# Kernel optimization log

Hardware: AMD Instinct MI355X
Metric: run time of the kernel (lower is better)

The kernel has to match this reference:

```python
import jax, jax.numpy as jnp
import numpy as np

B, S, D = 4, 4096, 768
E, SLOTS = 16, 1  # n_experts, slots_per_expert
H = 4 * D


def setup_inputs() -> dict:
    key = jax.random.key(0)
    k = jax.random.split(key, 6)
    scale1 = 1.0 / np.sqrt(D)
    scale2 = 1.0 / np.sqrt(H)
    return {
        "x": jax.random.normal(k[0], (B, S, D), dtype=jnp.float32),
        "phi": jax.random.normal(k[1], (D, E * SLOTS), dtype=jnp.float32),
        "W1": jax.random.normal(k[2], (E, D, H), dtype=jnp.float32) * scale1,
        "b1": jnp.zeros((E, H), dtype=jnp.float32),
        "W2": jax.random.normal(k[3], (E, H, D), dtype=jnp.float32) * scale2,
        "b2": jnp.zeros((E, D), dtype=jnp.float32),
    }


def reference(x, phi, W1, b1, W2, b2):
    # logits: [B, S, E*SLOTS]
    logits = jnp.einsum("bsd,dn->bsn", x, phi)
    dispatch_weights = jax.nn.softmax(logits, axis=-1)  # over slots
    combine_weights = jax.nn.softmax(logits, axis=1)    # over sequence
    # xs: [B, E*SLOTS, D] = dispatch^T @ x
    xs = jnp.einsum("bsn,bsd->bnd", dispatch_weights, x)
    xs = xs.reshape(B, E, SLOTS, D)
    # per-expert FFN, batched over experts: GELU (exact, as torch nn.GELU default)
    h = jnp.einsum("bepd,edh->beph", xs, W1) + b1[None, :, None, :]
    h = jax.nn.gelu(h, approximate=False)
    ys = jnp.einsum("beph,ehd->bepd", h, W2) + b2[None, :, None, :]
    ys = ys.reshape(B, E * SLOTS, D)
    # combine: [B, S, D]
    y = jnp.einsum("bsn,bnd->bsd", combine_weights, ys)
    return y
```

## Files before the change

kernel.cpp:

```cpp
#include <hip/hip_runtime.h>
#include <math.h>

constexpr int B = 4, S = 4096, D = 768, E = 16, N = 16, H = 3072;
constexpr int SCH = 32;
constexpr int NSCH = S / SCH;
constexpr int HL = 96;
constexpr int NHC = H / HL;
constexpr int LBLK = 32;
constexpr int LPB = S / LBLK;

constexpr size_t OFF_LOG  = 0;
constexpr size_t OFF_DW   = OFF_LOG + (size_t)B * S * N;
constexpr size_t OFF_PCM  = OFF_DW + (size_t)B * S * N;
constexpr size_t OFF_PCS  = OFF_PCM + (size_t)B * LPB * N;
constexpr size_t OFF_CMAX = OFF_PCS + (size_t)B * LPB * N;
constexpr size_t OFF_CSUM = OFF_CMAX + (size_t)B * N;
constexpr size_t OFF_XSP  = OFF_CSUM + (size_t)B * N;
constexpr size_t OFF_XS   = OFF_XSP + (size_t)B * NSCH * N * D;
constexpr size_t OFF_YSP  = OFF_XS + (size_t)B * N * D;
constexpr size_t OFF_YS   = OFF_YSP + (size_t)NHC * B * E * D;

__device__ __forceinline__ void fma4(float4& a, float s, const float4& w) {
    a.x = fmaf(s, w.x, a.x);
    a.y = fmaf(s, w.y, a.y);
    a.z = fmaf(s, w.z, a.z);
    a.w = fmaf(s, w.w, a.w);
}

__global__ __launch_bounds__(256) void k_logits(const float* __restrict__ x,
                                                const float* __restrict__ phi,
                                                float* __restrict__ logits,
                                                float* __restrict__ dw,
                                                float* __restrict__ pcm,
                                                float* __restrict__ pcs) {
    __shared__ float ph[16][D];
    __shared__ float rm[16][16], rs[16][16];
    const int t = threadIdx.x;
    const int blk = blockIdx.x;
    const int b = blk / LPB;
    const int s0 = (blk % LPB) * LBLK;

#pragma unroll
    for (int i = 0; i < 12; ++i) {
        const int idx = i * 1024 + t * 4;
        const float4 v = *reinterpret_cast<const float4*>(phi + idx);
        const int d0 = idx >> 4;
        const int n0 = idx & 15;
        ph[n0 + 0][d0] = v.x;
        ph[n0 + 1][d0] = v.y;
        ph[n0 + 2][d0] = v.z;
        ph[n0 + 3][d0] = v.w;
    }
    __syncthreads();

    const int gid = t >> 4;
    const int ln = t & 15;
    const int s = s0 + gid * 2;
    const float* xr0 = x + ((size_t)b * S + s) * D;
    const float* xr1 = xr0 + D;

    float4 a0[12], a1[12];
#pragma unroll
    for (int j = 0; j < 12; ++j) {
        a0[j] = *reinterpret_cast<const float4*>(xr0 + j * 64 + ln * 4);
        a1[j] = *reinterpret_cast<const float4*>(xr1 + j * 64 + ln * 4);
    }
    float p0[16], p1[16];
#pragma unroll
    for (int n = 0; n < 16; ++n) {
        float q0 = 0.f, q1 = 0.f;
#pragma unroll
        for (int j = 0; j < 12; ++j) {
            const float4 pv = *reinterpret_cast<const float4*>(&ph[n][j * 64 + ln * 4]);
            q0 = fmaf(a0[j].x, pv.x, q0); q1 = fmaf(a1[j].x, pv.x, q1);
            q0 = fmaf(a0[j].y, pv.y, q0); q1 = fmaf(a1[j].y, pv.y, q1);
            q0 = fmaf(a0[j].z, pv.z, q0); q1 = fmaf(a1[j].z, pv.z, q1);
            q0 = fmaf(a0[j].w, pv.w, q0); q1 = fmaf(a1[j].w, pv.w, q1);
        }
        p0[n] = q0; p1[n] = q1;
    }
#pragma unroll
    for (int m = 1; m < 16; m <<= 1) {
#pragma unroll
        for (int n = 0; n < 16; ++n) {
            p0[n] += __shfl_xor(p0[n], m, 64);
            p1[n] += __shfl_xor(p1[n], m, 64);
        }
    }
    float m0 = -1e30f, m1 = -1e30f;
#pragma unroll
    for (int n = 0; n < 16; ++n) { m0 = fmaxf(m0, p0[n]); m1 = fmaxf(m1, p1[n]); }
    float su0 = 0.f, su1 = 0.f;
#pragma unroll
    for (int n = 0; n < 16; ++n) { su0 += __expf(p0[n] - m0); su1 += __expf(p1[n] - m1); }
    const size_t o0 = ((size_t)b * S + s) * N + ln;
    logits[o0] = p0[ln];
    logits[o0 + N] = p1[ln];
    dw[o0] = __expf(p0[ln] - m0) / su0;
    dw[o0 + N] = __expf(p1[ln] - m1) / su1;

    const float mm = fmaxf(p0[ln], p1[ln]);
    const float ss = __expf(p0[ln] - mm) + __expf(p1[ln] - mm);
    rm[gid][ln] = mm;
    rs[gid][ln] = ss;
    __syncthreads();
    if (t < 16) {
        float M = -1e30f;
#pragma unroll
        for (int g = 0; g < 16; ++g) M = fmaxf(M, rm[g][t]);
        float SS = 0.f;
#pragma unroll
        for (int g = 0; g < 16; ++g) SS += rs[g][t] * __expf(rm[g][t] - M);
        pcm[blk * 16 + t] = M;
        pcs[blk * 16 + t] = SS;
    }
}

__global__ __launch_bounds__(192) void k_xsp(const float* __restrict__ x,
                                             const float* __restrict__ dw,
                                             float* __restrict__ xsp) {
    const int blk = blockIdx.x;
    const int b = blk / NSCH;
    const int c = blk % NSCH;
    const int t = threadIdx.x;
    const int d = t * 4;
    float4 a[16];
#pragma unroll
    for (int n = 0; n < 16; ++n) a[n] = float4{0.f, 0.f, 0.f, 0.f};
    const float* xb = x + ((size_t)b * S + (size_t)c * SCH) * D + d;
    const float* dwb = dw + ((size_t)b * S + (size_t)c * SCH) * N;
#pragma unroll 2
    for (int s = 0; s < SCH; ++s) {
        const float4 xv = *reinterpret_cast<const float4*>(xb + (size_t)s * D);
#pragma unroll
        for (int n = 0; n < 16; ++n) {
            const float w = dwb[s * N + n];
            a[n].x = fmaf(w, xv.x, a[n].x);
            a[n].y = fmaf(w, xv.y, a[n].y);
            a[n].z = fmaf(w, xv.z, a[n].z);
            a[n].w = fmaf(w, xv.w, a[n].w);
        }
    }
    float* o = xsp + (size_t)blk * N * D + d;
#pragma unroll
    for (int n = 0; n < 16; ++n)
        *reinterpret_cast<float4*>(o + (size_t)n * D) = a[n];
}

__global__ __launch_bounds__(256) void k_xsred_cmerge(const float* __restrict__ xsp,
                                                      float* __restrict__ xs,
                                                      const float* __restrict__ pcm,
                                                      const float* __restrict__ pcs,
                                                      float* __restrict__ cmax,
                                                      float* __restrict__ csum) {
    const int t = threadIdx.x;
    if (blockIdx.x < 192) {
        const int i = blockIdx.x * 256 + t;
        const int b = i / (N * D);
        const int rem = i % (N * D);
        const float* p = xsp + (size_t)b * NSCH * N * D + rem;
        float sum = 0.f;
#pragma unroll 4
        for (int c = 0; c < NSCH; ++c) sum += p[(size_t)c * N * D];
        xs[i] = sum;
    } else if (t < 64) {
        const int b = t >> 4, n = t & 15;
        float M = -1e30f;
#pragma unroll 8
        for (int c = 0; c < LPB; ++c) M = fmaxf(M, pcm[((size_t)b * LPB + c) * 16 + n]);
        float SS = 0.f;
#pragma unroll 8
        for (int c = 0; c < LPB; ++c)
            SS += pcs[((size_t)b * LPB + c) * 16 + n] * __expf(pcm[((size_t)b * LPB + c) * 16 + n] - M);
        cmax[b * 16 + n] = M;
        csum[b * 16 + n] = SS;
    }
}

__global__ __launch_bounds__(384) void k_ffn(const float* __restrict__ xs,
                                             const float* __restrict__ W1,
                                             const float* __restrict__ b1,
                                             const float* __restrict__ W2,
                                             float* __restrict__ ysp) {
    __shared__ __align__(16) float xs_lds[D][4];
    __shared__ __align__(16) float red_lds[16][HL][4];
    __shared__ __align__(16) float h_lds[HL][4];

    const int t = threadIdx.x;
    const int e = blockIdx.x / NHC;
    const int hc = blockIdx.x % NHC;
    const int h0 = hc * HL;

    for (int idx = t; idx < D; idx += 384) {
#pragma unroll
        for (int b = 0; b < 4; ++b)
            xs_lds[idx][b] = xs[((size_t)b * N + e) * D + idx];
    }
    __syncthreads();

    {
        const int c4 = (t % 24) * 4;
        const int q = t / 24;
        float4 h0a{0,0,0,0}, h1a{0,0,0,0}, h2a{0,0,0,0}, h3a{0,0,0,0};
        const float* w1p = W1 + ((size_t)e * D + (size_t)q * 48) * H + h0 + c4;
#pragma unroll 8
        for (int dd = 0; dd < 48; ++dd) {
            const float4 w = *reinterpret_cast<const float4*>(w1p + (size_t)dd * H);
            const float* xv = &xs_lds[q * 48 + dd][0];
            const float x0 = xv[0], x1 = xv[1], x2 = xv[2], x3 = xv[3];
            h0a.x = fmaf(x0, w.x, h0a.x); h0a.y = fmaf(x0, w.y, h0a.y);
            h0a.z = fmaf(x0, w.z, h0a.z); h0a.w = fmaf(x0, w.w, h0a.w);
            h1a.x = fmaf(x1, w.x, h1a.x); h1a.y = fmaf(x1, w.y, h1a.y);
            h1a.z = fmaf(x1, w.z, h1a.z); h1a.w = fmaf(x1, w.w, h1a.w);
            h2a.x = fmaf(x2, w.x, h2a.x); h2a.y = fmaf(x2, w.y, h2a.y);
            h2a.z = fmaf(x2, w.z, h2a.z); h2a.w = fmaf(x2, w.w, h2a.w);
            h3a.x = fmaf(x3, w.x, h3a.x); h3a.y = fmaf(x3, w.y, h3a.y);
            h3a.z = fmaf(x3, w.z, h3a.z); h3a.w = fmaf(x3, w.w, h3a.w);
        }
        *reinterpret_cast<float4*>(&red_lds[q][c4 + 0][0]) = float4{h0a.x, h1a.x, h2a.x, h3a.x};
        *reinterpret_cast<float4*>(&red_lds[q][c4 + 1][0]) = float4{h0a.y, h1a.y, h2a.y, h3a.y};
        *reinterpret_cast<float4*>(&red_lds[q][c4 + 2][0]) = float4{h0a.z, h1a.z, h2a.z, h3a.z};
        *reinterpret_cast<float4*>(&red_lds[q][c4 + 3][0]) = float4{h0a.w, h1a.w, h2a.w, h3a.w};
    }
    __syncthreads();

    const int dgrp = t % 192;
    const int kq = t / 192;
    const float* w2p = W2 + ((size_t)e * H + h0 + (size_t)kq * 48) * D + dgrp * 4;
    float4 wpre[8];
#pragma unroll
    for (int i = 0; i < 8; ++i)
        wpre[i] = *reinterpret_cast<const float4*>(w2p + (size_t)i * D);

    {
        const int col = t >> 2, b = t & 3;
        float s = 0.f;
#pragma unroll
        for (int q = 0; q < 16; ++q) s += red_lds[q][col][b];
        s += b1[(size_t)e * H + h0 + col];
        s = 0.5f * s * (1.0f + erff(s * 0.70710678118654752f));
        h_lds[col][b] = s;
    }
    __syncthreads();

    float4 acc[4];
#pragma unroll
    for (int b = 0; b < 4; ++b) acc[b] = float4{0.f, 0.f, 0.f, 0.f};

#pragma unroll
    for (int kk = 0; kk < 8; ++kk) {
        const float4 hv = *reinterpret_cast<const float4*>(&h_lds[kq * 48 + kk][0]);
        fma4(acc[0], hv.x, wpre[kk]);
        fma4(acc[1], hv.y, wpre[kk]);
        fma4(acc[2], hv.z, wpre[kk]);
        fma4(acc[3], hv.w, wpre[kk]);
    }
#pragma unroll 8
    for (int kk = 8; kk < 48; ++kk) {
        const float4 w = *reinterpret_cast<const float4*>(w2p + (size_t)kk * D);
        const float4 hv = *reinterpret_cast<const float4*>(&h_lds[kq * 48 + kk][0]);
        fma4(acc[0], hv.x, w);
        fma4(acc[1], hv.y, w);
        fma4(acc[2], hv.z, w);
        fma4(acc[3], hv.w, w);
    }

    float4* pbuf = reinterpret_cast<float4*>(&xs_lds[0][0]);
    __syncthreads();
    if (kq == 1) {
#pragma unroll
        for (int b = 0; b < 4; ++b) pbuf[dgrp * 4 + b] = acc[b];
    }
    __syncthreads();
    if (kq == 0) {
#pragma unroll
        for (int b = 0; b < 4; ++b) {
            const float4 u = pbuf[dgrp * 4 + b];
            float4 r{acc[b].x + u.x, acc[b].y + u.y, acc[b].z + u.z, acc[b].w + u.w};
            *reinterpret_cast<float4*>(ysp + (((size_t)hc * B + b) * E + e) * D + dgrp * 4) = r;
        }
    }
}

__global__ __launch_bounds__(256) void k_ysred(const float* __restrict__ ysp,
                                               const float* __restrict__ b2,
                                               float* __restrict__ ys) {
    const int i4 = blockIdx.x * 256 + threadIdx.x;
    const int rem4 = i4 % (E * D / 4);
    float4 v = *reinterpret_cast<const float4*>(b2 + (size_t)rem4 * 4);
#pragma unroll 8
    for (int p = 0; p < NHC; ++p) {
        const float4 u = *reinterpret_cast<const float4*>(ysp + (size_t)p * B * E * D + (size_t)i4 * 4);
        v.x += u.x; v.y += u.y; v.z += u.z; v.w += u.w;
    }
    *reinterpret_cast<float4*>(ys + (size_t)i4 * 4) = v;
}

__global__ __launch_bounds__(192) void k_combine(const float* __restrict__ logits,
                                                 const float* __restrict__ cmax,
                                                 const float* __restrict__ csum,
                                                 const float* __restrict__ ys,
                                                 float* __restrict__ y) {
    const int blk = blockIdx.x;
    const int b = blk / (S / 8);
    const int s0 = (blk % (S / 8)) * 8;
    const int t = threadIdx.x;
    const int d4 = t * 4;

    float4 ysr[16];
    float cm[16], ci[16];
#pragma unroll
    for (int n = 0; n < 16; ++n) {
        ysr[n] = *reinterpret_cast<const float4*>(ys + ((size_t)b * N + n) * D + d4);
        cm[n] = cmax[b * N + n];
        ci[n] = 1.0f / csum[b * N + n];
    }
#pragma unroll
    for (int r = 0; r < 8; ++r) {
        const int s = s0 + r;
        const float* lrow = logits + ((size_t)b * S + s) * N;
        float4 acc{0, 0, 0, 0};
#pragma unroll
        for (int n = 0; n < 16; ++n) {
            const float cw = __expf(lrow[n] - cm[n]) * ci[n];
            acc.x = fmaf(cw, ysr[n].x, acc.x);
            acc.y = fmaf(cw, ysr[n].y, acc.y);
            acc.z = fmaf(cw, ysr[n].z, acc.z);
            acc.w = fmaf(cw, ysr[n].w, acc.w);
        }
        *reinterpret_cast<float4*>(y + ((size_t)b * S + s) * D + d4) = acc;
    }
}

extern "C" void kernel_launch(void* const* d_in, const int* in_sizes, int n_in,
                              void* d_out, int out_size, void* d_ws, size_t ws_size,
                              hipStream_t stream) {
    const float* x   = (const float*)d_in[0];
    const float* phi = (const float*)d_in[1];
    const float* W1  = (const float*)d_in[2];
    const float* b1  = (const float*)d_in[3];
    const float* W2  = (const float*)d_in[4];
    const float* b2  = (const float*)d_in[5];
    float* y = (float*)d_out;
    float* ws = (float*)d_ws;

    float* logits = ws + OFF_LOG;
    float* dw     = ws + OFF_DW;
    float* pcm    = ws + OFF_PCM;
    float* pcs    = ws + OFF_PCS;
    float* cmax   = ws + OFF_CMAX;
    float* csum   = ws + OFF_CSUM;
    float* xsp    = ws + OFF_XSP;
    float* xs     = ws + OFF_XS;
    float* ysp    = ws + OFF_YSP;
    float* ys     = ws + OFF_YS;

    k_logits<<<B * LPB, 256, 0, stream>>>(x, phi, logits, dw, pcm, pcs);
    k_xsp<<<B * NSCH, 192, 0, stream>>>(x, dw, xsp);
    k_xsred_cmerge<<<193, 256, 0, stream>>>(xsp, xs, pcm, pcs, cmax, csum);
    k_ffn<<<E * NHC, 384, 0, stream>>>(xs, W1, b1, W2, ysp);
    k_ysred<<<48, 256, 0, stream>>>(ysp, b2, ys);
    k_combine<<<B * (S / 8), 192, 0, stream>>>(logits, cmax, csum, ys, y);
}
```

Before: 153.8 us.

## Fuse logits and dispatch-weighted x reduction into one kernel; restructure FFN thread mapping

Merges the logits/softmax kernel with the per-chunk dispatch^T·x reduction. Each block stages its 32 rows of x in LDS and keeps the dispatch weights there, so x is read from global memory once instead of twice and the dw buffer round trip is removed. It also remaps the FFN kernel so each thread computes two column groups over a shorter K slice, using a 32-way reduction in phase 1 and a 4-way reduction in phase 2. The cost is a large LDS footprint in the fused kernel (about 150 KB) and idle threads during the xsp phase, which may reduce occupancy.

```diff
diff --git a/kernel.cpp b/kernel.cpp
--- a/kernel.cpp
+++ b/kernel.cpp
@@ -2,21 +2,18 @@
 #include <math.h>
 
 constexpr int B = 4, S = 4096, D = 768, E = 16, N = 16, H = 3072;
-constexpr int SCH = 32;
-constexpr int NSCH = S / SCH;
 constexpr int HL = 96;
 constexpr int NHC = H / HL;
 constexpr int LBLK = 32;
 constexpr int LPB = S / LBLK;
 
 constexpr size_t OFF_LOG  = 0;
-constexpr size_t OFF_DW   = OFF_LOG + (size_t)B * S * N;
-constexpr size_t OFF_PCM  = OFF_DW + (size_t)B * S * N;
+constexpr size_t OFF_PCM  = OFF_LOG + (size_t)B * S * N;
 constexpr size_t OFF_PCS  = OFF_PCM + (size_t)B * LPB * N;
 constexpr size_t OFF_CMAX = OFF_PCS + (size_t)B * LPB * N;
 constexpr size_t OFF_CSUM = OFF_CMAX + (size_t)B * N;
 constexpr size_t OFF_XSP  = OFF_CSUM + (size_t)B * N;
-constexpr size_t OFF_XS   = OFF_XSP + (size_t)B * NSCH * N * D;
+constexpr size_t OFF_XS   = OFF_XSP + (size_t)B * LPB * N * D;
 constexpr size_t OFF_YSP  = OFF_XS + (size_t)B * N * D;
 constexpr size_t OFF_YS   = OFF_YSP + (size_t)NHC * B * E * D;
 
@@ -27,13 +24,15 @@
     a.w = fmaf(s, w.w, a.w);
 }
 
-__global__ __launch_bounds__(256) void k_logits(const float* __restrict__ x,
-                                                const float* __restrict__ phi,
-                                                float* __restrict__ logits,
-                                                float* __restrict__ dw,
-                                                float* __restrict__ pcm,
-                                                float* __restrict__ pcs) {
+__global__ __launch_bounds__(256) void k_lx(const float* __restrict__ x,
+                                            const float* __restrict__ phi,
+                                            float* __restrict__ logits,
+                                            float* __restrict__ xsp,
+                                            float* __restrict__ pcm,
+                                            float* __restrict__ pcs) {
     __shared__ float ph[16][D];
+    __shared__ float xr[LBLK][D + 4];
+    __shared__ float dwl[LBLK][16];
     __shared__ float rm[16][16], rs[16][16];
     const int t = threadIdx.x;
     const int blk = blockIdx.x;
@@ -51,19 +50,25 @@
         ph[n0 + 2][d0] = v.z;
         ph[n0 + 3][d0] = v.w;
     }
+    const float* xsrc = x + ((size_t)b * S + s0) * D;
+#pragma unroll
+    for (int i = 0; i < 24; ++i) {
+        const int idx = i * 256 + t;
+        const int r = idx / 192, c = idx % 192;
+        *reinterpret_cast<float4*>(&xr[r][c * 4]) =
+            *reinterpret_cast<const float4*>(xsrc + (size_t)idx * 4);
+    }
     __syncthreads();
 
     const int gid = t >> 4;
     const int ln = t & 15;
-    const int s = s0 + gid * 2;
-    const float* xr0 = x + ((size_t)b * S + s) * D;
-    const float* xr1 = xr0 + D;
+    const int r0 = gid * 2, r1 = r0 + 1;
 
     float4 a0[12], a1[12];
 #pragma unroll
     for (int j = 0; j < 12; ++j) {
-        a0[j] = *reinterpret_cast<const float4*>(xr0 + j * 64 + ln * 4);
-        a1[j] = *reinterpret_cast<const float4*>(xr1 + j * 64 + ln * 4);
+        a0[j] = *reinterpret_cast<const float4*>(&xr[r0][j * 64 + ln * 4]);
+        a1[j] = *reinterpret_cast<const float4*>(&xr[r1][j * 64 + ln * 4]);
     }
     float p0[16], p1[16];
 #pragma unroll
@@ -93,17 +98,17 @@
     float su0 = 0.f, su1 = 0.f;
 #pragma unroll
     for (int n = 0; n < 16; ++n) { su0 += __expf(p0[n] - m0); su1 += __expf(p1[n] - m1); }
-    const size_t o0 = ((size_t)b * S + s) * N + ln;
+    const size_t o0 = ((size_t)b * S + s0 + r0) * N + ln;
     logits[o0] = p0[ln];
     logits[o0 + N] = p1[ln];
-    dw[o0] = __expf(p0[ln] - m0) / su0;
-    dw[o0 + N] = __expf(p1[ln] - m1) / su1;
+    dwl[r0][ln] = __expf(p0[ln] - m0) / su0;
+    dwl[r1][ln] = __expf(p1[ln] - m1) / su1;
 
     const float mm = fmaxf(p0[ln], p1[ln]);
-    const float ss = __expf(p0[ln] - mm) + __expf(p1[ln] - mm);
     rm[gid][ln] = mm;
-    rs[gid][ln] = ss;
-    __syncthreads();
+    rs[gid][ln] = __expf(p0[ln] - mm) + __expf(p1[ln] - mm);
+    __syncthreads();
+
     if (t < 16) {
         float M = -1e30f;
 #pragma unroll
@@ -114,37 +119,29 @@
         pcm[blk * 16 + t] = M;
         pcs[blk * 16 + t] = SS;
     }
-}
-
-__global__ __launch_bounds__(192) void k_xsp(const float* __restrict__ x,
-                                             const float* __restrict__ dw,
-                                             float* __restrict__ xsp) {
-    const int blk = blockIdx.x;
-    const int b = blk / NSCH;
-    const int c = blk % NSCH;
-    const int t = threadIdx.x;
-    const int d = t * 4;
-    float4 a[16];
-#pragma unroll
-    for (int n = 0; n < 16; ++n) a[n] = float4{0.f, 0.f, 0.f, 0.f};
-    const float* xb = x + ((size_t)b * S + (size_t)c * SCH) * D + d;
-    const float* dwb = dw + ((size_t)b * S + (size_t)c * SCH) * N;
-#pragma unroll 2
-    for (int s = 0; s < SCH; ++s) {
-        const float4 xv = *reinterpret_cast<const float4*>(xb + (size_t)s * D);
-#pragma unroll
-        for (int n = 0; n < 16; ++n) {
-            const float w = dwb[s * N + n];
-            a[n].x = fmaf(w, xv.x, a[n].x);
-            a[n].y = fmaf(w, xv.y, a[n].y);
-            a[n].z = fmaf(w, xv.z, a[n].z);
-            a[n].w = fmaf(w, xv.w, a[n].w);
-        }
-    }
-    float* o = xsp + (size_t)blk * N * D + d;
-#pragma unroll
-    for (int n = 0; n < 16; ++n)
-        *reinterpret_cast<float4*>(o + (size_t)n * D) = a[n];
+
+    if (t < 192) {
+        const int d4 = t * 4;
+        float4 a[16];
+#pragma unroll
+        for (int n = 0; n < 16; ++n) a[n] = float4{0.f, 0.f, 0.f, 0.f};
+#pragma unroll 4
+        for (int s = 0; s < LBLK; ++s) {
+            const float4 xv = *reinterpret_cast<const float4*>(&xr[s][d4]);
+#pragma unroll
+            for (int n = 0; n < 16; ++n) {
+                const float w = dwl[s][n];
+                a[n].x = fmaf(w, xv.x, a[n].x);
+                a[n].y = fmaf(w, xv.y, a[n].y);
+                a[n].z = fmaf(w, xv.z, a[n].z);
+                a[n].w = fmaf(w, xv.w, a[n].w);
+            }
+        }
+        float* o = xsp + (size_t)blk * N * D + d4;
+#pragma unroll
+        for (int n = 0; n < 16; ++n)
+            *reinterpret_cast<float4*>(o + (size_t)n * D) = a[n];
+    }
 }
 
 __global__ __launch_bounds__(256) void k_xsred_cmerge(const float* __restrict__ xsp,
@@ -158,10 +155,10 @@
         const int i = blockIdx.x * 256 + t;
         const int b = i / (N * D);
         const int rem = i % (N * D);
-        const float* p = xsp + (size_t)b * NSCH * N * D + rem;
+        const float* p = xsp + (size_t)b * LPB * N * D + rem;
         float sum = 0.f;
 #pragma unroll 4
-        for (int c = 0; c < NSCH; ++c) sum += p[(size_t)c * N * D];
+        for (int c = 0; c < LPB; ++c) sum += p[(size_t)c * N * D];
         xs[i] = sum;
     } else if (t < 64) {
         const int b = t >> 4, n = t & 15;
@@ -183,7 +180,7 @@
                                              const float* __restrict__ W2,
                                              float* __restrict__ ysp) {
     __shared__ __align__(16) float xs_lds[D][4];
-    __shared__ __align__(16) float red_lds[16][HL][4];
+    __shared__ __align__(16) float red[32][HL][4];
     __shared__ __align__(16) float h_lds[HL][4];
 
     const int t = threadIdx.x;
@@ -199,85 +196,92 @@
     __syncthreads();
 
     {
-        const int c4 = (t % 24) * 4;
-        const int q = t / 24;
-        float4 h0a{0,0,0,0}, h1a{0,0,0,0}, h2a{0,0,0,0}, h3a{0,0,0,0};
-        const float* w1p = W1 + ((size_t)e * D + (size_t)q * 48) * H + h0 + c4;
-#pragma unroll 8
-        for (int dd = 0; dd < 48; ++dd) {
-            const float4 w = *reinterpret_cast<const float4*>(w1p + (size_t)dd * H);
-            const float* xv = &xs_lds[q * 48 + dd][0];
+        const int q = t / 12;
+        const int cg = t % 12;
+        const int c4a = cg * 4, c4b = 48 + cg * 4;
+        float4 aA[4], aB[4];
+#pragma unroll
+        for (int b = 0; b < 4; ++b) { aA[b] = float4{0,0,0,0}; aB[b] = float4{0,0,0,0}; }
+        const float* w1p = W1 + ((size_t)e * D + (size_t)q * 24) * H + h0;
+#pragma unroll 8
+        for (int dd = 0; dd < 24; ++dd) {
+            const float* row = w1p + (size_t)dd * H;
+            const float4 wa = *reinterpret_cast<const float4*>(row + c4a);
+            const float4 wb = *reinterpret_cast<const float4*>(row + c4b);
+            const float* xv = &xs_lds[q * 24 + dd][0];
             const float x0 = xv[0], x1 = xv[1], x2 = xv[2], x3 = xv[3];
-            h0a.x = fmaf(x0, w.x, h0a.x); h0a.y = fmaf(x0, w.y, h0a.y);
-            h0a.z = fmaf(x0, w.z, h0a.z); h0a.w = fmaf(x0, w.w, h0a.w);
-            h1a.x = fmaf(x1, w.x, h1a.x); h1a.y = fmaf(x1, w.y, h1a.y);
-            h1a.z = fmaf(x1, w.z, h1a.z); h1a.w = fmaf(x1, w.w, h1a.w);
-            h2a.x = fmaf(x2, w.x, h2a.x); h2a.y = fmaf(x2, w.y, h2a.y);
-            h2a.z = fmaf(x2, w.z, h2a.z); h2a.w = fmaf(x2, w.w, h2a.w);
-            h3a.x = fmaf(x3, w.x, h3a.x); h3a.y = fmaf(x3, w.y, h3a.y);
-            h3a.z = fmaf(x3, w.z, h3a.z); h3a.w = fmaf(x3, w.w, h3a.w);
-        }
-        *reinterpret_cast<float4*>(&red_lds[q][c4 + 0][0]) = float4{h0a.x, h1a.x, h2a.x, h3a.x};
-        *reinterpret_cast<float4*>(&red_lds[q][c4 + 1][0]) = float4{h0a.y, h1a.y, h2a.y, h3a.y};
-        *reinterpret_cast<float4*>(&red_lds[q][c4 + 2][0]) = float4{h0a.z, h1a.z, h2a.z, h3a.z};
-        *reinterpret_cast<float4*>(&red_lds[q][c4 + 3][0]) = float4{h0a.w, h1a.w, h2a.w, h3a.w};
-    }
-    __syncthreads();
-
-    const int dgrp = t % 192;
-    const int kq = t / 192;
-    const float* w2p = W2 + ((size_t)e * H + h0 + (size_t)kq * 48) * D + dgrp * 4;
-    float4 wpre[8];
-#pragma unroll
-    for (int i = 0; i < 8; ++i)
-        wpre[i] = *reinterpret_cast<const float4*>(w2p + (size_t)i * D);
+            fma4(aA[0], x0, wa); fma4(aB[0], x0, wb);
+            fma4(aA[1], x1, wa); fma4(aB[1], x1, wb);
+            fma4(aA[2], x2, wa); fma4(aB[2], x2, wb);
+            fma4(aA[3], x3, wa); fma4(aB[3], x3, wb);
+        }
+        *reinterpret_cast<float4*>(&red[q][c4a + 0][0]) = float4{aA[0].x, aA[1].x, aA[2].x, aA[3].x};
+        *reinterpret_cast<float4*>(&red[q][c4a + 1][0]) = float4{aA[0].y, aA[1].y, aA[2].y, aA[3].y};
+        *reinterpret_cast<float4*>(&red[q][c4a + 2][0]) = float4{aA[0].z, aA[1].z, aA[2].z, aA[3].z};
+        *reinterpret_cast<float4*>(&red[q][c4a + 3][0]) = float4{aA[0].w, aA[1].w, aA[2].w, aA[3].w};
+        *reinterpret_cast<float4*>(&red[q][c4b + 0][0]) = float4{aB[0].x, aB[1].x, aB[2].x, aB[3].x};
+        *reinterpret_cast<float4*>(&red[q][c4b + 1][0]) = float4{aB[0].y, aB[1].y, aB[2].y, aB[3].y};
+        *reinterpret_cast<float4*>(&red[q][c4b + 2][0]) = float4{aB[0].z, aB[1].z, aB[2].z, aB[3].z};
+        *reinterpret_cast<float4*>(&red[q][c4b + 3][0]) = float4{aB[0].w, aB[1].w, aB[2].w, aB[3].w};
+    }
+    __syncthreads();
 
     {
         const int col = t >> 2, b = t & 3;
         float s = 0.f;
 #pragma unroll
-        for (int q = 0; q < 16; ++q) s += red_lds[q][col][b];
+        for (int q = 0; q < 32; ++q) s += red[q][col][b];
         s += b1[(size_t)e * H + h0 + col];
         s = 0.5f * s * (1.0f + erff(s * 0.70710678118654752f));
         h_lds[col][b] = s;
     }
     __syncthreads();
 
-    float4 acc[4];
-#pragma unroll
-    for (int b = 0; b < 4; ++b) acc[b] = float4{0.f, 0.f, 0.f, 0.f};
-
-#pragma unroll
-    for (int kk = 0; kk < 8; ++kk) {
-        const float4 hv = *reinterpret_cast<const float4*>(&h_lds[kq * 48 + kk][0]);
-        fma4(acc[0], hv.x, wpre[kk]);
-        fma4(acc[1], hv.y, wpre[kk]);
-        fma4(acc[2], hv.z, wpre[kk]);
-        fma4(acc[3], hv.w, wpre[kk]);
-    }
-#pragma unroll 8
-    for (int kk = 8; kk < 48; ++kk) {
-        const float4 w = *reinterpret_cast<const float4*>(w2p + (size_t)kk * D);
-        const float4 hv = *reinterpret_cast<const float4*>(&h_lds[kq * 48 + kk][0]);
-        fma4(acc[0], hv.x, w);
-        fma4(acc[1], hv.y, w);
-        fma4(acc[2], hv.z, w);
-        fma4(acc[3], hv.w, w);
-    }
-
-    float4* pbuf = reinterpret_cast<float4*>(&xs_lds[0][0]);
-    __syncthreads();
-    if (kq == 1) {
-#pragma unroll
-        for (int b = 0; b < 4; ++b) pbuf[dgrp * 4 + b] = acc[b];
+    const int kq = t / 96;
+    const int dg = t % 96;
+    const int d4a = dg * 4, d4b = 384 + dg * 4;
+    float4 yA[4], yB[4];
+#pragma unroll
+    for (int b = 0; b < 4; ++b) { yA[b] = float4{0,0,0,0}; yB[b] = float4{0,0,0,0}; }
+    {
+        const float* w2p = W2 + ((size_t)e * H + h0 + (size_t)kq * 24) * D;
+#pragma unroll 8
+        for (int kk = 0; kk < 24; ++kk) {
+            const float* row = w2p + (size_t)kk * D;
+            const float4 wa = *reinterpret_cast<const float4*>(row + d4a);
+            const float4 wb = *reinterpret_cast<const float4*>(row + d4b);
+            const float* hv = &h_lds[kq * 24 + kk][0];
+            fma4(yA[0], hv[0], wa); fma4(yB[0], hv[0], wb);
+            fma4(yA[1], hv[1], wa); fma4(yB[1], hv[1], wb);
+            fma4(yA[2], hv[2], wa); fma4(yB[2], hv[2], wb);
+            fma4(yA[3], hv[3], wa); fma4(yB[3], hv[3], wb);
+        }
+    }
+    float4* pb = reinterpret_cast<float4*>(&red[0][0][0]);
+    __syncthreads();
+    if (kq > 0) {
+        const int base = ((kq - 1) * 96 + dg) * 8;
+#pragma unroll
+        for (int b = 0; b < 4; ++b) {
+            pb[base + b * 2 + 0] = yA[b];
+            pb[base + b * 2 + 1] = yB[b];
+        }
     }
     __syncthreads();
     if (kq == 0) {
 #pragma unroll
         for (int b = 0; b < 4; ++b) {
-            const float4 u = pbuf[dgrp * 4 + b];
-            float4 r{acc[b].x + u.x, acc[b].y + u.y, acc[b].z + u.z, acc[b].w + u.w};
-            *reinterpret_cast<float4*>(ysp + (((size_t)hc * B + b) * E + e) * D + dgrp * 4) = r;
+            float4 rA = yA[b], rB = yB[b];
+#pragma unroll
+            for (int p = 0; p < 3; ++p) {
+                const int base = (p * 96 + dg) * 8 + b * 2;
+                const float4 uA = pb[base + 0], uB = pb[base + 1];
+                rA.x += uA.x; rA.y += uA.y; rA.z += uA.z; rA.w += uA.w;
+                rB.x += uB.x; rB.y += uB.y; rB.z += uB.z; rB.w += uB.w;
+            }
+            float* o = ysp + (((size_t)hc * B + b) * E + e) * D;
+            *reinterpret_cast<float4*>(o + d4a) = rA;
+            *reinterpret_cast<float4*>(o + d4b) = rB;
         }
     }
 }
@@ -345,7 +349,6 @@
     float* ws = (float*)d_ws;
 
     float* logits = ws + OFF_LOG;
-    float* dw     = ws + OFF_DW;
     float* pcm    = ws + OFF_PCM;
     float* pcs    = ws + OFF_PCS;
     float* cmax   = ws + OFF_CMAX;
@@ -355,8 +358,7 @@
     float* ysp    = ws + OFF_YSP;
     float* ys     = ws + OFF_YS;
 
-    k_logits<<<B * LPB, 256, 0, stream>>>(x, phi, logits, dw, pcm, pcs);
-    k_xsp<<<B * NSCH, 192, 0, stream>>>(x, dw, xsp);
+    k_lx<<<B * LPB, 256, 0, stream>>>(x, phi, logits, xsp, pcm, pcs);
     k_xsred_cmerge<<<193, 256, 0, stream>>>(xsp, xs, pcm, pcs, cmax, csum);
     k_ffn<<<E * NHC, 384, 0, stream>>>(xs, W1, b1, W2, ysp);
     k_ysred<<<48, 256, 0, stream>>>(ysp, b2, ys);
```

Result: no change. 154.1 us (+0.2%).
